# Performance work log

Hardware: AMD Instinct MI355X
Metric: run time of the kernel (lower is better)

## Reference

```python
import jax, jax.numpy as jnp
import numpy as np

TOP_K = 2

def setup_inputs() -> dict:
    key = jax.random.key(0)
    k1, k2 = jax.random.split(key)
    N, D, E = 16384, 2048, 64
    x = jax.random.normal(k1, (N, D), dtype=jnp.float32)
    W = jax.random.normal(k2, (D, E), dtype=jnp.float32) * (1.0 / np.sqrt(D))
    b = jnp.zeros((E,), dtype=jnp.float32)
    return {"x": x, "W": W, "b": b}

def reference(x, W, b):
    # gate linear: [N, D] @ [D, E] + [E]
    logits = jnp.einsum('nd,de->ne', x, W) + b
    gates = jax.nn.softmax(logits, axis=-1)
    topk_vals, topk_idx = jax.lax.top_k(gates, TOP_K)  # [N, k]
    N = gates.shape[0]
    rows = jnp.arange(N)[:, None]  # [N, 1] broadcast over k
    dispatch_mask = jnp.zeros_like(gates).at[rows, topk_idx].set(topk_vals)
    return dispatch_mask, topk_idx
```

## Files before the change

kernel.cpp:

```cpp
#include <hip/hip_runtime.h>
#include <math.h>

#define NROWS 16384
#define DDIM  2048
#define EEXP  64
#define RB    32
#define KC    64
#define NCH   (DDIM / KC)

#define LVL     8192
#define WBUF(b) ((b) * 24576)

typedef short  bf16x8 __attribute__((ext_vector_type(8)));
typedef float  f32x16 __attribute__((ext_vector_type(16)));

union V4 { uint4 u; bf16x8 s; };

static __device__ __forceinline__ void split3x2(float f0, float f1,
                                                unsigned int &p0, unsigned int &p1,
                                                unsigned int &p2) {
    unsigned int a0 = __float_as_uint(f0), b0 = __float_as_uint(f1);
    unsigned int ah = a0 & 0xffff0000u,   bh = b0 & 0xffff0000u;
    float fa1 = f0 - __uint_as_float(ah);
    float fb1 = f1 - __uint_as_float(bh);
    unsigned int a1 = __float_as_uint(fa1), b1 = __float_as_uint(fb1);
    unsigned int am = a1 & 0xffff0000u,     bm = b1 & 0xffff0000u;
    float fa2 = fa1 - __uint_as_float(am);
    float fb2 = fb1 - __uint_as_float(bm);
    p0 = (a0 >> 16) | bh;
    p1 = (a1 >> 16) | bm;
    p2 = (__float_as_uint(fa2) >> 16) | (__float_as_uint(fb2) & 0xffff0000u);
}

static __device__ __forceinline__ void cvt8(float4 u, float4 v, V4 &q0, V4 &q1, V4 &q2) {
    split3x2(u.x, u.y, q0.u.x, q1.u.x, q2.u.x);
    split3x2(u.z, u.w, q0.u.y, q1.u.y, q2.u.y);
    split3x2(v.x, v.y, q0.u.z, q1.u.z, q2.u.z);
    split3x2(v.z, v.w, q0.u.w, q1.u.w, q2.u.w);
}

#define MM(ACC, A, B) ACC = __builtin_amdgcn_mfma_f32_32x32x16_bf16((A), (B), ACC, 0, 0, 0)

__global__ __launch_bounds__(512, 4)
void router_kernel(const float* __restrict__ x,
                   const float* __restrict__ W,
                   const float* __restrict__ bias_v,
                   float* __restrict__ mask_out,
                   float* __restrict__ idx_out) {
    __shared__ __align__(16) unsigned char smem[49152];

    const int tid  = threadIdx.x;
    const int lane = tid & 63;
    const int w    = __builtin_amdgcn_readfirstlane(tid >> 6);
    const int kg   = w & 3;
    const int et   = w >> 2;
    const int row0 = blockIdx.x * RB;
    const int l31  = lane & 31;
    const int h    = lane >> 5;

    const float* xp = x + (size_t)(row0 + l31) * DDIM + kg * 16 + h * 8;

    const float* wq = W + (size_t)(w * 8) * EEXP + lane;
    const int wb = lane * 128 + ((w * 16) ^ ((lane & 7) << 4));

    const int rB = et * 32 + l31;
    const int be = rB * 128 + (((2 * kg + h) * 16) ^ ((rB & 7) << 4));

    f32x16 acc;
#pragma unroll
    for (int i = 0; i < 16; ++i) acc[i] = 0.f;

    float wr[8];
#pragma unroll
    for (int j = 0; j < 8; ++j) wr[j] = wq[(size_t)j * EEXP];
    {
        V4 q0, q1, q2;
        cvt8(make_float4(wr[0], wr[1], wr[2], wr[3]),
             make_float4(wr[4], wr[5], wr[6], wr[7]), q0, q1, q2);
        unsigned char* d = smem + WBUF(0);
        *(uint4*)(d + wb) = q0.u;
        *(uint4*)(d + LVL + wb) = q1.u;
        *(uint4*)(d + 2 * LVL + wb) = q2.u;
    }
    float4 xlo = *(const float4*)(xp);
    float4 xhi = *(const float4*)(xp + 4);
    __syncthreads();

#pragma unroll 1
    for (int c = 0; c < NCH; ++c) {
        const int  buf  = c & 1;
        const bool more = (c + 1) < NCH;

        if (more) {
            const float* q = wq + (size_t)(c + 1) * KC * EEXP;
#pragma unroll
            for (int j = 0; j < 8; ++j) wr[j] = q[(size_t)j * EEXP];
        }

        V4 a0, a1, a2;
        cvt8(xlo, xhi, a0, a1, a2);

        if (more) {
            xlo = *(const float4*)(xp + (c + 1) * KC);
            xhi = *(const float4*)(xp + (c + 1) * KC + 4);
        }

        const unsigned char* wB = smem + WBUF(buf);
        bf16x8 b0 = *(const bf16x8*)(wB + be);
        bf16x8 b1 = *(const bf16x8*)(wB + LVL + be);
        bf16x8 b2 = *(const bf16x8*)(wB + 2 * LVL + be);

        MM(acc, a0.s, b0);
        MM(acc, a0.s, b1);
        MM(acc, a1.s, b0);
        MM(acc, a0.s, b2);
        MM(acc, a1.s, b1);
        MM(acc, a2.s, b0);

        if (more) {
            V4 q0, q1, q2;
            cvt8(make_float4(wr[0], wr[1], wr[2], wr[3]),
                 make_float4(wr[4], wr[5], wr[6], wr[7]), q0, q1, q2);
            unsigned char* d = smem + WBUF(buf ^ 1);
            *(uint4*)(d + wb) = q0.u;
            *(uint4*)(d + LVL + wb) = q1.u;
            *(uint4*)(d + 2 * LVL + wb) = q2.u;
        }
        __syncthreads();
    }

    const float bias = bias_v[lane];
    float* ep = (float*)smem;
#pragma unroll
    for (int r = 0; r < 16; ++r) {
        const int rowl = (r & 3) + 8 * (r >> 2) + 4 * h;
        ep[kg * 2048 + rowl * 64 + et * 32 + l31] = acc[r];
    }
    __syncthreads();

#pragma unroll
    for (int rr = 0; rr < 4; ++rr) {
        const int rl  = w * 4 + rr;
        const int row = row0 + rl;
        float logit = bias + ep[rl * 64 + lane]
                           + ep[2048 + rl * 64 + lane]
                           + ep[4096 + rl * 64 + lane]
                           + ep[6144 + rl * 64 + lane];

        float m = logit;
#pragma unroll
        for (int off = 32; off >= 1; off >>= 1) m = fmaxf(m, __shfl_xor(m, off));
        float ex = __expf(logit - m);
        float s = ex;
#pragma unroll
        for (int off = 32; off >= 1; off >>= 1) s += __shfl_xor(s, off);
        float gate = ex / s;

        float v1 = logit; int i1 = lane;
#pragma unroll
        for (int off = 32; off >= 1; off >>= 1) {
            float ov = __shfl_xor(v1, off);
            int   oi = __shfl_xor(i1, off);
            if (ov > v1 || (ov == v1 && oi < i1)) { v1 = ov; i1 = oi; }
        }
        float v2 = (lane == i1) ? -INFINITY : logit; int i2 = lane;
#pragma unroll
        for (int off = 32; off >= 1; off >>= 1) {
            float ov = __shfl_xor(v2, off);
            int   oi = __shfl_xor(i2, off);
            if (ov > v2 || (ov == v2 && oi < i2)) { v2 = ov; i2 = oi; }
        }

        float outv = (lane == i1 || lane == i2) ? gate : 0.0f;
        mask_out[(size_t)row * EEXP + lane] = outv;
        if (lane == 0) {
            idx_out[row * 2 + 0] = (float)i1;
            idx_out[row * 2 + 1] = (float)i2;
        }
    }
}

extern "C" void kernel_launch(void* const* d_in, const int* in_sizes, int n_in,
                              void* d_out, int out_size, void* d_ws, size_t ws_size,
                              hipStream_t stream) {
    const float* x = (const float*)d_in[0];
    const float* W = (const float*)d_in[1];
    const float* b = (const float*)d_in[2];
    float* mask_out = (float*)d_out;
    float* idx_out  = mask_out + (size_t)NROWS * EEXP;

    dim3 grid(NROWS / RB);
    dim3 block(512);
    router_kernel<<<grid, block, 0, stream>>>(x, W, b, mask_out, idx_out);
}
```

Baseline: 218.0 us.

## Pre-split W into bf16x3 fragments once and stream them directly to registers

Adds a small pre-pass kernel that converts W into three-level bf16 split fragments, laid out in workspace in MFMA-operand order. The main kernel then loads B operands straight from global memory (L2-resident) into registers, removing the per-block W conversion, the LDS double buffer and the per-chunk __syncthreads. It also unrolls the loop by two chunks with a deeper prefetch and splits the work across two accumulators to break the MFMA dependency chain. The cost is an extra kernel launch, more global/L2 traffic for W per block, and higher register pressure.

```diff
diff --git a/kernel.cpp b/kernel.cpp
--- a/kernel.cpp
+++ b/kernel.cpp
@@ -8,8 +8,8 @@
 #define KC    64
 #define NCH   (DDIM / KC)
 
-#define LVL     8192
-#define WBUF(b) ((b) * 24576)
+#define WSPLIT_BYTES 786432
+#define CHSTRIDE     24576
 
 typedef short  bf16x8 __attribute__((ext_vector_type(8)));
 typedef float  f32x16 __attribute__((ext_vector_type(16)));
@@ -41,13 +41,41 @@
 
 #define MM(ACC, A, B) ACC = __builtin_amdgcn_mfma_f32_32x32x16_bf16((A), (B), ACC, 0, 0, 0)
 
+#define MM6(A0, A1, A2, B0, B1, B2)                                \
+    MM(accA, (A0).s, (B0).s); MM(accB, (A0).s, (B1).s);            \
+    MM(accA, (A1).s, (B0).s); MM(accB, (A0).s, (B2).s);            \
+    MM(accA, (A1).s, (B1).s); MM(accB, (A2).s, (B0).s);
+
+__global__ __launch_bounds__(256)
+void wsplit_kernel(const float* __restrict__ W, unsigned char* __restrict__ ws) {
+    const int t  = blockIdx.x * 256 + threadIdx.x;
+    const int e  = t & 63;
+    const int ko = t >> 6;
+    const int k0 = ko * 8;
+    float f[8];
+#pragma unroll
+    for (int j = 0; j < 8; ++j) f[j] = W[(size_t)(k0 + j) * EEXP + e];
+    V4 q0, q1, q2;
+    cvt8(make_float4(f[0], f[1], f[2], f[3]),
+         make_float4(f[4], f[5], f[6], f[7]), q0, q1, q2);
+    const int c  = k0 >> 6;
+    const int kg = (k0 >> 4) & 3;
+    const int h  = (k0 >> 3) & 1;
+    const int et = e >> 5;
+    const int ln = h * 32 + (e & 31);
+    unsigned char* d = ws + (size_t)(((((c * 4 + kg) * 2 + et) * 64) + ln) * 48);
+    *(uint4*)(d +  0) = q0.u;
+    *(uint4*)(d + 16) = q1.u;
+    *(uint4*)(d + 32) = q2.u;
+}
+
 __global__ __launch_bounds__(512, 4)
 void router_kernel(const float* __restrict__ x,
-                   const float* __restrict__ W,
+                   const unsigned char* __restrict__ wsplit,
                    const float* __restrict__ bias_v,
                    float* __restrict__ mask_out,
                    float* __restrict__ idx_out) {
-    __shared__ __align__(16) unsigned char smem[49152];
+    __shared__ __align__(16) float ep[8192];
 
     const int tid  = threadIdx.x;
     const int lane = tid & 63;
@@ -59,85 +87,61 @@
     const int h    = lane >> 5;
 
     const float* xp = x + (size_t)(row0 + l31) * DDIM + kg * 16 + h * 8;
+    const unsigned char* wp = wsplit + (size_t)(((kg * 2 + et) * 64 + lane) * 48);
 
-    const float* wq = W + (size_t)(w * 8) * EEXP + lane;
-    const int wb = lane * 128 + ((w * 16) ^ ((lane & 7) << 4));
+    f32x16 accA, accB;
+#pragma unroll
+    for (int i = 0; i < 16; ++i) { accA[i] = 0.f; accB[i] = 0.f; }
 
-    const int rB = et * 32 + l31;
-    const int be = rB * 128 + (((2 * kg + h) * 16) ^ ((rB & 7) << 4));
-
-    f32x16 acc;
-#pragma unroll
-    for (int i = 0; i < 16; ++i) acc[i] = 0.f;
-
-    float wr[8];
-#pragma unroll
-    for (int j = 0; j < 8; ++j) wr[j] = wq[(size_t)j * EEXP];
-    {
-        V4 q0, q1, q2;
-        cvt8(make_float4(wr[0], wr[1], wr[2], wr[3]),
-             make_float4(wr[4], wr[5], wr[6], wr[7]), q0, q1, q2);
-        unsigned char* d = smem + WBUF(0);
-        *(uint4*)(d + wb) = q0.u;
-        *(uint4*)(d + LVL + wb) = q1.u;
-        *(uint4*)(d + 2 * LVL + wb) = q2.u;
-    }
-    float4 xlo = *(const float4*)(xp);
-    float4 xhi = *(const float4*)(xp + 4);
-    __syncthreads();
+    float4 x0a = *(const float4*)(xp);
+    float4 x0b = *(const float4*)(xp + 4);
+    V4 b00, b01, b02, b10, b11, b12;
+    b00.u = *(const uint4*)(wp);
+    b01.u = *(const uint4*)(wp + 16);
+    b02.u = *(const uint4*)(wp + 32);
+    float4 x1a = *(const float4*)(xp + KC);
+    float4 x1b = *(const float4*)(xp + KC + 4);
+    b10.u = *(const uint4*)(wp + CHSTRIDE);
+    b11.u = *(const uint4*)(wp + CHSTRIDE + 16);
+    b12.u = *(const uint4*)(wp + CHSTRIDE + 32);
 
 #pragma unroll 1
-    for (int c = 0; c < NCH; ++c) {
-        const int  buf  = c & 1;
-        const bool more = (c + 1) < NCH;
-
-        if (more) {
-            const float* q = wq + (size_t)(c + 1) * KC * EEXP;
-#pragma unroll
-            for (int j = 0; j < 8; ++j) wr[j] = q[(size_t)j * EEXP];
+    for (int c = 0; c < NCH; c += 2) {
+        V4 a0, a1, a2;
+        cvt8(x0a, x0b, a0, a1, a2);
+        if (c + 2 < NCH) {
+            x0a = *(const float4*)(xp + (c + 2) * KC);
+            x0b = *(const float4*)(xp + (c + 2) * KC + 4);
         }
-
-        V4 a0, a1, a2;
-        cvt8(xlo, xhi, a0, a1, a2);
-
-        if (more) {
-            xlo = *(const float4*)(xp + (c + 1) * KC);
-            xhi = *(const float4*)(xp + (c + 1) * KC + 4);
+        MM6(a0, a1, a2, b00, b01, b02)
+        if (c + 2 < NCH) {
+            const unsigned char* q = wp + (size_t)(c + 2) * CHSTRIDE;
+            b00.u = *(const uint4*)(q);
+            b01.u = *(const uint4*)(q + 16);
+            b02.u = *(const uint4*)(q + 32);
         }
-
-        const unsigned char* wB = smem + WBUF(buf);
-        bf16x8 b0 = *(const bf16x8*)(wB + be);
-        bf16x8 b1 = *(const bf16x8*)(wB + LVL + be);
-        bf16x8 b2 = *(const bf16x8*)(wB + 2 * LVL + be);
-
-        MM(acc, a0.s, b0);
-        MM(acc, a0.s, b1);
-        MM(acc, a1.s, b0);
-        MM(acc, a0.s, b2);
-        MM(acc, a1.s, b1);
-        MM(acc, a2.s, b0);
-
-        if (more) {
-            V4 q0, q1, q2;
-            cvt8(make_float4(wr[0], wr[1], wr[2], wr[3]),
-                 make_float4(wr[4], wr[5], wr[6], wr[7]), q0, q1, q2);
-            unsigned char* d = smem + WBUF(buf ^ 1);
-            *(uint4*)(d + wb) = q0.u;
-            *(uint4*)(d + LVL + wb) = q1.u;
-            *(uint4*)(d + 2 * LVL + wb) = q2.u;
+        cvt8(x1a, x1b, a0, a1, a2);
+        if (c + 3 < NCH) {
+            x1a = *(const float4*)(xp + (c + 3) * KC);
+            x1b = *(const float4*)(xp + (c + 3) * KC + 4);
         }
-        __syncthreads();
+        MM6(a0, a1, a2, b10, b11, b12)
+        if (c + 3 < NCH) {
+            const unsigned char* q = wp + (size_t)(c + 3) * CHSTRIDE;
+            b10.u = *(const uint4*)(q);
+            b11.u = *(const uint4*)(q + 16);
+            b12.u = *(const uint4*)(q + 32);
+        }
     }
 
-    const float bias = bias_v[lane];
-    float* ep = (float*)smem;
 #pragma unroll
     for (int r = 0; r < 16; ++r) {
         const int rowl = (r & 3) + 8 * (r >> 2) + 4 * h;
-        ep[kg * 2048 + rowl * 64 + et * 32 + l31] = acc[r];
+        ep[kg * 2048 + rowl * 64 + et * 32 + l31] = accA[r] + accB[r];
     }
     __syncthreads();
 
+    const float bias = bias_v[lane];
 #pragma unroll
     for (int rr = 0; rr < 4; ++rr) {
         const int rl  = w * 4 + rr;
@@ -188,8 +192,8 @@
     const float* b = (const float*)d_in[2];
     float* mask_out = (float*)d_out;
     float* idx_out  = mask_out + (size_t)NROWS * EEXP;
+    unsigned char* ws = (unsigned char*)d_ws;
 
-    dim3 grid(NROWS / RB);
-    dim3 block(512);
-    router_kernel<<<grid, block, 0, stream>>>(x, W, b, mask_out, idx_out);
+    wsplit_kernel<<<dim3(64), dim3(256), 0, stream>>>(W, ws);
+    router_kernel<<<dim3(NROWS / RB), dim3(512), 0, stream>>>(x, ws, b, mask_out, idx_out);
 }
```

Measured after the change: 238.2 us. 1.09x slower.
